# Optimization experiments

Hardware: AMD Instinct MI355X
Metric: run time of the kernel (lower is better)

The kernel has to match this reference:

```python
import jax, jax.numpy as jnp
import numpy as np
from jax import lax

EPS = 1e-5

def binarize(x):
    # sign forward, straight-through (identity) backward, matching torch .data-trick Binarize
    return x + lax.stop_gradient(jnp.sign(x) - x)

def conv2d(x, w, pad):
    return lax.conv_general_dilated(x, w, window_strides=(1, 1),
                                    padding=[(pad, pad), (pad, pad)],
                                    dimension_numbers=('NCHW', 'OIHW', 'NCHW'))

def maxpool_k2s1(x):
    return lax.reduce_window(x, -jnp.inf, lax.max, (1, 1, 2, 2), (1, 1, 1, 1), 'VALID')

def batchnorm(x, g, b):
    # training-mode BN: batch statistics over (N, H, W)
    mean = jnp.mean(x, axis=(0, 2, 3), keepdims=True)
    var = jnp.var(x, axis=(0, 2, 3), keepdims=True)
    return (x - mean) * lax.rsqrt(var + EPS) * g[None, :, None, None] + b[None, :, None, None]

def hardtanh(x):
    return jnp.clip(x, -1.0, 1.0)

def setup_inputs() -> dict:
    key = jax.random.key(0)
    ks = jax.random.split(key, 11)
    B = 4096
    return {
        'x':   jax.random.normal(ks[0], (B, 12, 12, 15), jnp.float32),
        'w1':  jax.random.normal(ks[1], (48, 12, 3, 3), jnp.float32) * 0.1,
        'g1':  1.0 + 0.1 * jax.random.normal(ks[2], (48,), jnp.float32),
        'b1':  0.1 * jax.random.normal(ks[3], (48,), jnp.float32),
        'w2':  jax.random.normal(ks[4], (48, 48, 3, 3), jnp.float32) * 0.1,
        'g2':  1.0 + 0.1 * jax.random.normal(ks[5], (48,), jnp.float32),
        'b2':  0.1 * jax.random.normal(ks[6], (48,), jnp.float32),
        'w3':  jax.random.normal(ks[7], (48, 48, 3, 3), jnp.float32) * 0.1,
        'g3':  1.0 + 0.1 * jax.random.normal(ks[8], (48,), jnp.float32),
        'b3':  0.1 * jax.random.normal(ks[9], (48,), jnp.float32),
        'wfc': jax.random.normal(ks[10], (5, 54 * 48), jnp.float32) * 0.02,
    }

def reference(x, w1, g1, b1, w2, g2, b2, w3, g3, b3, wfc):
    # BinarizeConv2d binarizes activations (in_channels != 3) and weights; returns binarized input too
    xb1 = binarize(x)                                  # [B,12,12,15]
    h = conv2d(xb1, binarize(w1), pad=1)               # [B,48,12,15]
    h = maxpool_k2s1(h)                                # [B,48,11,14]
    h = hardtanh(batchnorm(h, g1, b1))
    xb2 = binarize(h)
    h = conv2d(xb2, binarize(w2), pad=0)               # [B,48,9,12]
    h = hardtanh(batchnorm(h, g2, b2))
    xb3 = binarize(h)
    h = conv2d(xb3, binarize(w3), pad=0)               # [B,48,7,10]
    h = maxpool_k2s1(h)                                # [B,48,6,9] -> 54 spatial
    h = hardtanh(batchnorm(h, g3, b3))
    f = h.reshape(h.shape[0], -1)                      # [B, 2592]
    fb = binarize(f)
    out = fb @ binarize(wfc).T                         # [B, 5]  (LogSoftmax defined but never applied)
    return (out, xb1, xb2, xb3, fb)
```

## Files before the change

### kernel.cpp

```cpp
#include <hip/hip_runtime.h>
#include <stdint.h>

typedef unsigned long long u64;
typedef unsigned short u16;


#define NB 4096

#define WS_STATS 0
#define WS_W1P   20480
#define WS_W2P   24576
#define WS_W3P   28672
#define WS_WFCP  32768
#define WS_A1    40960
#define WS_P1    5111808

#define OUT_OFF 0
#define XB1_OFF 20480
#define XB2_OFF 8867840
#define XB3_OFF 39145472
#define FB_OFF  60379136

__device__ __forceinline__ float fsign(float v) {
    return (v > 0.0f) ? 1.0f : ((v < 0.0f) ? -1.0f : 0.0f);
}

__global__ __launch_bounds__(512)
void kw_pack(const float* __restrict__ w1, const float* __restrict__ w2,
             const float* __restrict__ w3, const float* __restrict__ wfc,
             char* __restrict__ ws) {
    int t = threadIdx.x;
    long long* stats = (long long*)(ws + WS_STATS);
    for (int i = t; i < 2304; i += 512) stats[i] = 0;
    if (t < 432) {
        int oc = t / 9, p = t % 9;
        u16 m1 = 0;
        for (int c = 0; c < 12; ++c)
            if (w1[oc*108 + c*9 + p] > 0.0f) m1 |= (u16)(1u << c);
        ((u16*)(ws + WS_W1P))[t] = m1;
        u64 m2 = 0, m3 = 0;
        for (int c = 0; c < 48; ++c) {
            if (w2[oc*432 + c*9 + p] > 0.0f) m2 |= (1ull << c);
            if (w3[oc*432 + c*9 + p] > 0.0f) m3 |= (1ull << c);
        }
        ((u64*)(ws + WS_W2P))[t] = m2;
        ((u64*)(ws + WS_W3P))[t] = m3;
    }
    if (t < 205) {
        int o = t / 41, j = t % 41;
        u64 m = 0;
        for (int l = 0; l < 64; ++l) {
            int k = j*64 + l;
            if (k < 2592 && wfc[o*2592 + k] > 0.0f) m |= (1ull << l);
        }
        ((u64*)(ws + WS_WFCP))[t] = m;
    }
}

__global__ __launch_bounds__(256)
void k0_binx(const float* __restrict__ x, float* __restrict__ dout,
             char* __restrict__ ws) {
    int id = blockIdx.x*256 + threadIdx.x;
    int b = id / 45, s4 = id % 45;
    const float4* xp = (const float4*)(x + b*2160);
    float4* op = (float4*)(dout + XB1_OFF + (size_t)b*2160);
    u16 m0 = 0, m1 = 0, m2 = 0, m3 = 0;
    #pragma unroll
    for (int c = 0; c < 12; ++c) {
        float4 v = xp[c*45 + s4];
        float4 o;
        o.x = fsign(v.x); o.y = fsign(v.y); o.z = fsign(v.z); o.w = fsign(v.w);
        op[c*45 + s4] = o;
        u16 bit = (u16)(1u << c);
        if (v.x > 0.0f) m0 |= bit;
        if (v.y > 0.0f) m1 |= bit;
        if (v.z > 0.0f) m2 |= bit;
        if (v.w > 0.0f) m3 |= bit;
    }
    ushort4 mm; mm.x = m0; mm.y = m1; mm.z = m2; mm.w = m3;
    *((ushort4*)((u16*)(ws + WS_A1) + b*180 + s4*4)) = mm;
}

__global__ __launch_bounds__(192)
void k1_conv1(char* __restrict__ ws) {
    __shared__ u16 As[180];
    __shared__ signed char cmap[8640];
    __shared__ signed char pl[7392];
    int t = threadIdx.x, b = blockIdx.x;
    const u16* A1 = (const u16*)(ws + WS_A1) + b*180;
    if (t < 180) As[t] = A1[t];
    const u16* __restrict__ W1g = (const u16*)(ws + WS_W1P);
    __syncthreads();
    if (t < 180) {
        int y = t / 15, xx = t % 15;
        u16 tap[9], msk[9];
        int nv = 0;
        #pragma unroll
        for (int ky = 0; ky < 3; ++ky) {
            #pragma unroll
            for (int kx = 0; kx < 3; ++kx) {
                int yy = y + ky - 1, xc = xx + kx - 1;
                bool v = (yy >= 0 && yy < 12 && xc >= 0 && xc < 15);
                int yl = min(max(yy, 0), 11), xl = min(max(xc, 0), 14);
                tap[ky*3+kx] = As[yl*15 + xl];
                msk[ky*3+kx] = v ? (u16)0xFFFF : (u16)0;
                nv += v ? 12 : 0;
            }
        }
        for (int oc = 0; oc < 48; ++oc) {
            int acc = 0;
            #pragma unroll
            for (int k = 0; k < 9; ++k)
                acc += __popc((unsigned)((u16)(tap[k] ^ W1g[oc*9 + k]) & msk[k]));
            cmap[oc*180 + t] = (signed char)(nv - 2*acc);
        }
    }
    __syncthreads();
    signed char* gp = (signed char*)(ws + WS_P1) + (size_t)b*7392;
    for (int i = t; i < 7392; i += 192) {
        int c = i / 154, s = i % 154, py = s / 14, px = s % 14;
        int base = c*180 + py*15 + px;
        int mx = max(max((int)cmap[base],    (int)cmap[base+1]),
                     max((int)cmap[base+15], (int)cmap[base+16]));
        pl[i] = (signed char)mx;
        gp[i] = (signed char)mx;
    }
    __syncthreads();
    int wv = t >> 6, ln = t & 63, slot = b & 7;
    u64* st = (u64*)(ws + WS_STATS);
    for (int c = wv; c < 48; c += 3) {
        int sum = 0, sq = 0;
        for (int s = ln; s < 154; s += 64) {
            int v = pl[c*154 + s];
            sum += v; sq += v*v;
        }
        #pragma unroll
        for (int off = 32; off >= 1; off >>= 1) {
            sum += __shfl_down(sum, off);
            sq  += __shfl_down(sq, off);
        }
        if (ln == 0) {
            atomicAdd(&st[c*8 + slot],        (u64)(long long)sum);
            atomicAdd(&st[(48 + c)*8 + slot], (u64)(long long)sq);
        }
    }
}

__global__ __launch_bounds__(128)
void kA_bn1conv2(const float* __restrict__ g1, const float* __restrict__ b1,
                 float* __restrict__ dout, char* __restrict__ ws) {
    __shared__ float sc[48], sh[48];
    __shared__ int sm_i[1848];
    __shared__ u64 As[154];
    __shared__ short c2s[5184];
    signed char* sm = (signed char*)sm_i;
    int t = threadIdx.x, b = blockIdx.x;
    const int* gp = (const int*)(ws + WS_P1 + (size_t)b*7392);
    for (int i4 = t; i4 < 1848; i4 += 128) sm_i[i4] = gp[i4];
    const u64* __restrict__ W2g = (const u64*)(ws + WS_W2P);
    if (t < 48) {
        const long long* st = (const long long*)(ws + WS_STATS);
        long long s = 0, q = 0;
        #pragma unroll
        for (int k = 0; k < 8; ++k) { s += st[t*8 + k]; q += st[(48 + t)*8 + k]; }
        double N = 630784.0;
        double mean = (double)s / N;
        double var  = (double)q / N - mean*mean;
        double scale = (double)g1[t] / sqrt(var + 1e-5);
        sc[t] = (float)scale;
        sh[t] = (float)((double)b1[t] - mean*scale);
    }
    __syncthreads();
    float4* xo = (float4*)(dout + XB2_OFF + (size_t)b*7392);
    for (int i4 = t; i4 < 1848; i4 += 128) {
        int pv = sm_i[i4];
        int i = i4*4;
        float4 o;
        int c0 = i/154, c1 = (i+1)/154, c2i = (i+2)/154, c3 = (i+3)/154;
        o.x = fsign(sc[c0]*(float)(signed char)(pv)        + sh[c0]);
        o.y = fsign(sc[c1]*(float)(signed char)(pv >> 8)   + sh[c1]);
        o.z = fsign(sc[c2i]*(float)(signed char)(pv >> 16) + sh[c2i]);
        o.w = fsign(sc[c3]*(float)(signed char)(pv >> 24)  + sh[c3]);
        xo[i4] = o;
    }
    u64* A2g = (u64*)(ws + WS_A1) + (size_t)b*154;
    for (int s = t; s < 154; s += 128) {
        u64 m = 0;
        #pragma unroll
        for (int c = 0; c < 48; ++c)
            if (sc[c]*(float)sm[c*154 + s] + sh[c] > 0.0f) m |= (1ull << c);
        As[s] = m;
        A2g[s] = m;
    }
    __syncthreads();
    if (t < 108) {
        int oy = t / 12, ox = t % 12;
        u64 tap[9];
        #pragma unroll
        for (int ky = 0; ky < 3; ++ky)
            #pragma unroll
            for (int kx = 0; kx < 3; ++kx)
                tap[ky*3+kx] = As[(oy+ky)*14 + ox + kx];
        for (int oc = 0; oc < 48; ++oc) {
            int acc = 0;
            #pragma unroll
            for (int k = 0; k < 9; ++k)
                acc += __popcll(tap[k] ^ W2g[oc*9 + k]);
            c2s[oc*108 + t] = (short)(432 - 2*acc);
        }
    }
    __syncthreads();
    int wv = t >> 6, ln = t & 63, slot = b & 7;
    u64* st = (u64*)(ws + WS_STATS);
    for (int c = wv; c < 48; c += 2) {
        int sum = 0, sq = 0;
        for (int s = ln; s < 108; s += 64) {
            int v = c2s[c*108 + s];
            sum += v; sq += v*v;
        }
        #pragma unroll
        for (int off = 32; off >= 1; off >>= 1) {
            sum += __shfl_down(sum, off);
            sq  += __shfl_down(sq, off);
        }
        if (ln == 0) {
            atomicAdd(&st[(96 + c)*8 + slot],  (u64)(long long)sum);
            atomicAdd(&st[(144 + c)*8 + slot], (u64)(long long)sq);
        }
    }
}

__global__ __launch_bounds__(128)
void kB_bn2conv3(const float* __restrict__ g2, const float* __restrict__ b2,
                 float* __restrict__ dout, char* __restrict__ ws) {
    __shared__ float sc[48], sh[48];
    __shared__ u64 As[154];
    __shared__ short c2s[5184];
    __shared__ u64 A3[108];
    __shared__ short cm[3360];
    __shared__ short pls[2592];
    int t = threadIdx.x, b = blockIdx.x;
    const u64* A2g = (const u64*)(ws + WS_A1) + (size_t)b*154;
    for (int s = t; s < 154; s += 128) As[s] = A2g[s];
    const u64* __restrict__ W2g = (const u64*)(ws + WS_W2P);
    const u64* __restrict__ W3g = (const u64*)(ws + WS_W3P);
    if (t < 48) {
        const long long* st = (const long long*)(ws + WS_STATS);
        long long s = 0, q = 0;
        #pragma unroll
        for (int k = 0; k < 8; ++k) { s += st[(96 + t)*8 + k]; q += st[(144 + t)*8 + k]; }
        double N = 442368.0;
        double mean = (double)s / N;
        double var  = (double)q / N - mean*mean;
        double scale = (double)g2[t] / sqrt(var + 1e-5);
        sc[t] = (float)scale;
        sh[t] = (float)((double)b2[t] - mean*scale);
    }
    __syncthreads();
    if (t < 108) {
        int oy = t / 12, ox = t % 12;
        u64 tap[9];
        #pragma unroll
        for (int ky = 0; ky < 3; ++ky)
            #pragma unroll
            for (int kx = 0; kx < 3; ++kx)
                tap[ky*3+kx] = As[(oy+ky)*14 + ox + kx];
        for (int oc = 0; oc < 48; ++oc) {
            int acc = 0;
            #pragma unroll
            for (int k = 0; k < 9; ++k)
                acc += __popcll(tap[k] ^ W2g[oc*9 + k]);
            c2s[oc*108 + t] = (short)(432 - 2*acc);
        }
    }
    __syncthreads();
    float4* xo = (float4*)(dout + XB3_OFF + (size_t)b*5184);
    for (int i4 = t; i4 < 1296; i4 += 128) {
        int c = i4 / 27, s4 = i4 % 27;
        short4 v4 = *(const short4*)&c2s[c*108 + s4*4];
        float4 o;
        o.x = fsign(sc[c]*(float)v4.x + sh[c]);
        o.y = fsign(sc[c]*(float)v4.y + sh[c]);
        o.z = fsign(sc[c]*(float)v4.z + sh[c]);
        o.w = fsign(sc[c]*(float)v4.w + sh[c]);
        xo[i4] = o;
    }
    if (t < 108) {
        u64 m = 0;
        #pragma unroll
        for (int c = 0; c < 48; ++c)
            if (sc[c]*(float)c2s[c*108 + t] + sh[c] > 0.0f) m |= (1ull << c);
        A3[t] = m;
    }
    __syncthreads();
    if (t < 70) {
        int oy = t / 10, ox = t % 10;
        u64 tap[9];
        #pragma unroll
        for (int ky = 0; ky < 3; ++ky)
            #pragma unroll
            for (int kx = 0; kx < 3; ++kx)
                tap[ky*3+kx] = A3[(oy+ky)*12 + ox + kx];
        for (int oc = 0; oc < 48; ++oc) {
            int acc = 0;
            #pragma unroll
            for (int k = 0; k < 9; ++k)
                acc += __popcll(tap[k] ^ W3g[oc*9 + k]);
            cm[oc*70 + t] = (short)(432 - 2*acc);
        }
    }
    __syncthreads();
    short* p3g = (short*)(ws + WS_P1) + (size_t)b*2592;
    for (int i = t; i < 2592; i += 128) {
        int c = i / 54, s = i % 54, py = s / 9, px = s % 9;
        int base = c*70 + py*10 + px;
        int mx = max(max((int)cm[base],    (int)cm[base+1]),
                     max((int)cm[base+10], (int)cm[base+11]));
        pls[i] = (short)mx;
        p3g[i] = (short)mx;
    }
    __syncthreads();
    int wv = t >> 6, ln = t & 63, slot = b & 7;
    u64* st = (u64*)(ws + WS_STATS);
    for (int c = wv; c < 48; c += 2) {
        int sum = 0, sq = 0;
        if (ln < 54) {
            int v = pls[c*54 + ln];
            sum = v; sq = v*v;
        }
        #pragma unroll
        for (int off = 32; off >= 1; off >>= 1) {
            sum += __shfl_down(sum, off);
            sq  += __shfl_down(sq, off);
        }
        if (ln == 0) {
            atomicAdd(&st[(192 + c)*8 + slot], (u64)(long long)sum);
            atomicAdd(&st[(240 + c)*8 + slot], (u64)(long long)sq);
        }
    }
}

__global__ __launch_bounds__(256)
void kC_fbfc(const float* __restrict__ g3, const float* __restrict__ b3,
             float* __restrict__ dout, char* __restrict__ ws) {
    __shared__ float sc[48], sh[48];
    __shared__ short4 sm4[648];
    __shared__ unsigned char nib[648];
    __shared__ u64 fbb[41];
    short* sm = (short*)sm4;
    int t = threadIdx.x, b = blockIdx.x;
    const short4* p3 = (const short4*)((const short*)(ws + WS_P1) + (size_t)b*2592);
    for (int i4 = t; i4 < 648; i4 += 256) sm4[i4] = p3[i4];
    if (t < 48) {
        const long long* st = (const long long*)(ws + WS_STATS);
        long long s = 0, q = 0;
        #pragma unroll
        for (int k = 0; k < 8; ++k) { s += st[(192 + t)*8 + k]; q += st[(240 + t)*8 + k]; }
        double N = 221184.0;
        double mean = (double)s / N;
        double var  = (double)q / N - mean*mean;
        double scale = (double)g3[t] / sqrt(var + 1e-5);
        sc[t] = (float)scale;
        sh[t] = (float)((double)b3[t] - mean*scale);
    }
    __syncthreads();
    float4* fo = (float4*)(dout + FB_OFF + (size_t)b*2592);
    for (int i4 = t; i4 < 648; i4 += 256) {
        int i = i4*4;
        float4 o;
        unsigned n = 0;
        int c0 = i/54, c1 = (i+1)/54, c2 = (i+2)/54, c3 = (i+3)/54;
        float v0 = sc[c0]*(float)sm[i]   + sh[c0];
        float v1 = sc[c1]*(float)sm[i+1] + sh[c1];
        float v2 = sc[c2]*(float)sm[i+2] + sh[c2];
        float v3 = sc[c3]*(float)sm[i+3] + sh[c3];
        o.x = fsign(v0); o.y = fsign(v1); o.z = fsign(v2); o.w = fsign(v3);
        if (v0 > 0.0f) n |= 1u;
        if (v1 > 0.0f) n |= 2u;
        if (v2 > 0.0f) n |= 4u;
        if (v3 > 0.0f) n |= 8u;
        fo[i4] = o;
        nib[i4] = (unsigned char)n;
    }
    __syncthreads();
    if (t < 41) {
        u64 m = 0;
        #pragma unroll
        for (int k = 0; k < 16; ++k) {
            int j = t*16 + k;
            if (j < 648) m |= ((u64)nib[j]) << (4*k);
        }
        fbb[t] = m;
    }
    __syncthreads();
    if (t < 5) {
        const u64* Wf = (const u64*)(ws + WS_WFCP) + t*41;
        int acc = 0;
        #pragma unroll
        for (int j = 0; j < 41; ++j) acc += __popcll(fbb[j] ^ Wf[j]);
        dout[OUT_OFF + b*5 + t] = (float)(2592 - 2*acc);
    }
}

extern "C" void kernel_launch(void* const* d_in, const int* in_sizes, int n_in,
                              void* d_out, int out_size, void* d_ws, size_t ws_size,
                              hipStream_t stream) {
    const float* x   = (const float*)d_in[0];
    const float* w1  = (const float*)d_in[1];
    const float* g1  = (const float*)d_in[2];
    const float* b1  = (const float*)d_in[3];
    const float* w2  = (const float*)d_in[4];
    const float* g2  = (const float*)d_in[5];
    const float* b2  = (const float*)d_in[6];
    const float* w3  = (const float*)d_in[7];
    const float* g3  = (const float*)d_in[8];
    const float* b3  = (const float*)d_in[9];
    const float* wfc = (const float*)d_in[10];
    float* out = (float*)d_out;
    char* ws = (char*)d_ws;

    hipLaunchKernelGGL(kw_pack,     dim3(1),    dim3(512), 0, stream, w1, w2, w3, wfc, ws);
    hipLaunchKernelGGL(k0_binx,     dim3(720),  dim3(256), 0, stream, x, out, ws);
    hipLaunchKernelGGL(k1_conv1,    dim3(NB),   dim3(192), 0, stream, ws);
    hipLaunchKernelGGL(kA_bn1conv2, dim3(NB),   dim3(128), 0, stream, g1, b1, out, ws);
    hipLaunchKernelGGL(kB_bn2conv3, dim3(NB),   dim3(128), 0, stream, g2, b2, out, ws);
    hipLaunchKernelGGL(kC_fbfc,     dim3(NB),   dim3(256), 0, stream, g3, b3, out, ws);
}
```

Measured before the change: 768.5 us.

## Hoist BN constants to tiny kernels, widen blocks, split conv channels across threads

The per-block batch-norm scale/shift computation is moved into separate single-block kernels that write constants to workspace, so each of the 4096 blocks only loads 96 floats instead of redoing double-precision reductions. Conv2/conv3 blocks grow to 256 threads, with output channels split across two or three thread groups so more lanes do popcount work. Pooled outputs are packed and stored as int/int4 words instead of bytes/shorts, and the oc loops get unroll hints. This adds three extra kernel launches and higher per-block register and thread use, which may lower occupancy.

```diff
diff --git a/kernel.cpp b/kernel.cpp
--- a/kernel.cpp
+++ b/kernel.cpp
@@ -4,10 +4,10 @@
 typedef unsigned long long u64;
 typedef unsigned short u16;
 
-
 #define NB 4096
 
 #define WS_STATS 0
+#define WS_CONST 18432
 #define WS_W1P   20480
 #define WS_W2P   24576
 #define WS_W3P   28672
@@ -28,23 +28,23 @@
 __global__ __launch_bounds__(512)
 void kw_pack(const float* __restrict__ w1, const float* __restrict__ w2,
              const float* __restrict__ w3, const float* __restrict__ wfc,
-             char* __restrict__ ws) {
+             u16* __restrict__ W1P, u64* __restrict__ W2P, u64* __restrict__ W3P,
+             u64* __restrict__ WFCP, long long* __restrict__ stats) {
     int t = threadIdx.x;
-    long long* stats = (long long*)(ws + WS_STATS);
     for (int i = t; i < 2304; i += 512) stats[i] = 0;
     if (t < 432) {
         int oc = t / 9, p = t % 9;
         u16 m1 = 0;
         for (int c = 0; c < 12; ++c)
             if (w1[oc*108 + c*9 + p] > 0.0f) m1 |= (u16)(1u << c);
-        ((u16*)(ws + WS_W1P))[t] = m1;
+        W1P[t] = m1;
         u64 m2 = 0, m3 = 0;
         for (int c = 0; c < 48; ++c) {
             if (w2[oc*432 + c*9 + p] > 0.0f) m2 |= (1ull << c);
             if (w3[oc*432 + c*9 + p] > 0.0f) m3 |= (1ull << c);
         }
-        ((u64*)(ws + WS_W2P))[t] = m2;
-        ((u64*)(ws + WS_W3P))[t] = m3;
+        W2P[t] = m2;
+        W3P[t] = m3;
     }
     if (t < 205) {
         int o = t / 41, j = t % 41;
@@ -53,13 +53,30 @@
             int k = j*64 + l;
             if (k < 2592 && wfc[o*2592 + k] > 0.0f) m |= (1ull << l);
         }
-        ((u64*)(ws + WS_WFCP))[t] = m;
+        WFCP[t] = m;
+    }
+}
+
+__global__ __launch_bounds__(64)
+void kbn(const float* __restrict__ g, const float* __restrict__ bb,
+         const long long* __restrict__ st, float* __restrict__ cst, float Nf) {
+    int t = threadIdx.x;
+    if (t < 48) {
+        long long s = 0, q = 0;
+        #pragma unroll
+        for (int k = 0; k < 8; ++k) { s += st[t*8 + k]; q += st[(48 + t)*8 + k]; }
+        double N = (double)Nf;
+        double mean = (double)s / N;
+        double var  = (double)q / N - mean*mean;
+        double scale = (double)g[t] / sqrt(var + 1e-5);
+        cst[t]      = (float)scale;
+        cst[48 + t] = (float)((double)bb[t] - mean*scale);
     }
 }
 
 __global__ __launch_bounds__(256)
 void k0_binx(const float* __restrict__ x, float* __restrict__ dout,
-             char* __restrict__ ws) {
+             u16* __restrict__ A1) {
     int id = blockIdx.x*256 + threadIdx.x;
     int b = id / 45, s4 = id % 45;
     const float4* xp = (const float4*)(x + b*2160);
@@ -78,18 +95,19 @@
         if (v.w > 0.0f) m3 |= bit;
     }
     ushort4 mm; mm.x = m0; mm.y = m1; mm.z = m2; mm.w = m3;
-    *((ushort4*)((u16*)(ws + WS_A1) + b*180 + s4*4)) = mm;
+    *((ushort4*)(A1 + b*180 + s4*4)) = mm;
 }
 
 __global__ __launch_bounds__(192)
-void k1_conv1(char* __restrict__ ws) {
+void k1_conv1(const u16* __restrict__ W1, const u16* __restrict__ A1,
+              int* __restrict__ P1, u64* __restrict__ stats) {
     __shared__ u16 As[180];
-    __shared__ signed char cmap[8640];
-    __shared__ signed char pl[7392];
+    __shared__ int cmap_i[2160];
+    __shared__ int pl_i[1848];
+    signed char* cmap = (signed char*)cmap_i;
+    signed char* pl = (signed char*)pl_i;
     int t = threadIdx.x, b = blockIdx.x;
-    const u16* A1 = (const u16*)(ws + WS_A1) + b*180;
-    if (t < 180) As[t] = A1[t];
-    const u16* __restrict__ W1g = (const u16*)(ws + WS_W1P);
+    if (t < 180) As[t] = A1[b*180 + t];
     __syncthreads();
     if (t < 180) {
         int y = t / 15, xx = t % 15;
@@ -107,27 +125,33 @@
                 nv += v ? 12 : 0;
             }
         }
+        #pragma unroll 4
         for (int oc = 0; oc < 48; ++oc) {
             int acc = 0;
             #pragma unroll
             for (int k = 0; k < 9; ++k)
-                acc += __popc((unsigned)((u16)(tap[k] ^ W1g[oc*9 + k]) & msk[k]));
+                acc += __popc((unsigned)((u16)(tap[k] ^ W1[oc*9 + k]) & msk[k]));
             cmap[oc*180 + t] = (signed char)(nv - 2*acc);
         }
     }
     __syncthreads();
-    signed char* gp = (signed char*)(ws + WS_P1) + (size_t)b*7392;
-    for (int i = t; i < 7392; i += 192) {
-        int c = i / 154, s = i % 154, py = s / 14, px = s % 14;
-        int base = c*180 + py*15 + px;
-        int mx = max(max((int)cmap[base],    (int)cmap[base+1]),
-                     max((int)cmap[base+15], (int)cmap[base+16]));
-        pl[i] = (signed char)mx;
-        gp[i] = (signed char)mx;
+    int* gp = P1 + (size_t)b*1848;
+    for (int i4 = t; i4 < 1848; i4 += 192) {
+        int r = 0;
+        #pragma unroll
+        for (int u = 0; u < 4; ++u) {
+            int i = i4*4 + u;
+            int c = i / 154, s = i % 154, py = s / 14, px = s % 14;
+            int base = c*180 + py*15 + px;
+            int mx = max(max((int)cmap[base],    (int)cmap[base+1]),
+                         max((int)cmap[base+15], (int)cmap[base+16]));
+            r |= (mx & 0xff) << (8*u);
+        }
+        pl_i[i4] = r;
+        gp[i4] = r;
     }
     __syncthreads();
     int wv = t >> 6, ln = t & 63, slot = b & 7;
-    u64* st = (u64*)(ws + WS_STATS);
     for (int c = wv; c < 48; c += 3) {
         int sum = 0, sq = 0;
         for (int s = ln; s < 154; s += 64) {
@@ -140,39 +164,29 @@
             sq  += __shfl_down(sq, off);
         }
         if (ln == 0) {
-            atomicAdd(&st[c*8 + slot],        (u64)(long long)sum);
-            atomicAdd(&st[(48 + c)*8 + slot], (u64)(long long)sq);
-        }
-    }
-}
-
-__global__ __launch_bounds__(128)
-void kA_bn1conv2(const float* __restrict__ g1, const float* __restrict__ b1,
-                 float* __restrict__ dout, char* __restrict__ ws) {
+            atomicAdd((u64*)&stats[c*8 + slot],        (u64)(long long)sum);
+            atomicAdd((u64*)&stats[(48 + c)*8 + slot], (u64)(long long)sq);
+        }
+    }
+}
+
+__global__ __launch_bounds__(256)
+void kA_bn1conv2(const float* __restrict__ cst, const int4* __restrict__ P1,
+                 float* __restrict__ dout, u64* __restrict__ A2,
+                 const u64* __restrict__ W2, u64* __restrict__ stats) {
     __shared__ float sc[48], sh[48];
     __shared__ int sm_i[1848];
     __shared__ u64 As[154];
     __shared__ short c2s[5184];
     signed char* sm = (signed char*)sm_i;
     int t = threadIdx.x, b = blockIdx.x;
-    const int* gp = (const int*)(ws + WS_P1 + (size_t)b*7392);
-    for (int i4 = t; i4 < 1848; i4 += 128) sm_i[i4] = gp[i4];
-    const u64* __restrict__ W2g = (const u64*)(ws + WS_W2P);
-    if (t < 48) {
-        const long long* st = (const long long*)(ws + WS_STATS);
-        long long s = 0, q = 0;
-        #pragma unroll
-        for (int k = 0; k < 8; ++k) { s += st[t*8 + k]; q += st[(48 + t)*8 + k]; }
-        double N = 630784.0;
-        double mean = (double)s / N;
-        double var  = (double)q / N - mean*mean;
-        double scale = (double)g1[t] / sqrt(var + 1e-5);
-        sc[t] = (float)scale;
-        sh[t] = (float)((double)b1[t] - mean*scale);
-    }
+    const int4* gp = P1 + (size_t)b*462;
+    for (int i = t; i < 462; i += 256) ((int4*)sm_i)[i] = gp[i];
+    if (t < 48) sc[t] = cst[t];
+    else if (t < 96) sh[t - 48] = cst[t];
     __syncthreads();
     float4* xo = (float4*)(dout + XB2_OFF + (size_t)b*7392);
-    for (int i4 = t; i4 < 1848; i4 += 128) {
+    for (int i4 = t; i4 < 1848; i4 += 256) {
         int pv = sm_i[i4];
         int i = i4*4;
         float4 o;
@@ -183,36 +197,37 @@
         o.w = fsign(sc[c3]*(float)(signed char)(pv >> 24)  + sh[c3]);
         xo[i4] = o;
     }
-    u64* A2g = (u64*)(ws + WS_A1) + (size_t)b*154;
-    for (int s = t; s < 154; s += 128) {
+    if (t < 154) {
         u64 m = 0;
         #pragma unroll
         for (int c = 0; c < 48; ++c)
-            if (sc[c]*(float)sm[c*154 + s] + sh[c] > 0.0f) m |= (1ull << c);
-        As[s] = m;
-        A2g[s] = m;
-    }
-    __syncthreads();
-    if (t < 108) {
-        int oy = t / 12, ox = t % 12;
+            if (sc[c]*(float)sm[c*154 + t] + sh[c] > 0.0f) m |= (1ull << c);
+        As[t] = m;
+        A2[(size_t)b*154 + t] = m;
+    }
+    __syncthreads();
+    if (t < 216) {
+        int pos = (t < 108) ? t : (t - 108);
+        int ocb = (t < 108) ? 0 : 24;
+        int oy = pos / 12, ox = pos % 12;
         u64 tap[9];
         #pragma unroll
         for (int ky = 0; ky < 3; ++ky)
             #pragma unroll
             for (int kx = 0; kx < 3; ++kx)
                 tap[ky*3+kx] = As[(oy+ky)*14 + ox + kx];
-        for (int oc = 0; oc < 48; ++oc) {
+        #pragma unroll 4
+        for (int oc = ocb; oc < ocb + 24; ++oc) {
             int acc = 0;
             #pragma unroll
             for (int k = 0; k < 9; ++k)
-                acc += __popcll(tap[k] ^ W2g[oc*9 + k]);
-            c2s[oc*108 + t] = (short)(432 - 2*acc);
+                acc += __popcll(tap[k] ^ W2[oc*9 + k]);
+            c2s[oc*108 + pos] = (short)(432 - 2*acc);
         }
     }
     __syncthreads();
     int wv = t >> 6, ln = t & 63, slot = b & 7;
-    u64* st = (u64*)(ws + WS_STATS);
-    for (int c = wv; c < 48; c += 2) {
+    for (int c = wv; c < 48; c += 4) {
         int sum = 0, sq = 0;
         for (int s = ln; s < 108; s += 64) {
             int v = c2s[c*108 + s];
@@ -224,15 +239,17 @@
             sq  += __shfl_down(sq, off);
         }
         if (ln == 0) {
-            atomicAdd(&st[(96 + c)*8 + slot],  (u64)(long long)sum);
-            atomicAdd(&st[(144 + c)*8 + slot], (u64)(long long)sq);
-        }
-    }
-}
-
-__global__ __launch_bounds__(128)
-void kB_bn2conv3(const float* __restrict__ g2, const float* __restrict__ b2,
-                 float* __restrict__ dout, char* __restrict__ ws) {
+            atomicAdd((u64*)&stats[(96 + c)*8 + slot],  (u64)(long long)sum);
+            atomicAdd((u64*)&stats[(144 + c)*8 + slot], (u64)(long long)sq);
+        }
+    }
+}
+
+__global__ __launch_bounds__(256)
+void kB_bn2conv3(const float* __restrict__ cst, const u64* __restrict__ A2,
+                 const u64* __restrict__ W2, const u64* __restrict__ W3,
+                 float* __restrict__ dout, short* __restrict__ P3,
+                 u64* __restrict__ stats) {
     __shared__ float sc[48], sh[48];
     __shared__ u64 As[154];
     __shared__ short c2s[5184];
@@ -240,42 +257,32 @@
     __shared__ short cm[3360];
     __shared__ short pls[2592];
     int t = threadIdx.x, b = blockIdx.x;
-    const u64* A2g = (const u64*)(ws + WS_A1) + (size_t)b*154;
-    for (int s = t; s < 154; s += 128) As[s] = A2g[s];
-    const u64* __restrict__ W2g = (const u64*)(ws + WS_W2P);
-    const u64* __restrict__ W3g = (const u64*)(ws + WS_W3P);
-    if (t < 48) {
-        const long long* st = (const long long*)(ws + WS_STATS);
-        long long s = 0, q = 0;
-        #pragma unroll
-        for (int k = 0; k < 8; ++k) { s += st[(96 + t)*8 + k]; q += st[(144 + t)*8 + k]; }
-        double N = 442368.0;
-        double mean = (double)s / N;
-        double var  = (double)q / N - mean*mean;
-        double scale = (double)g2[t] / sqrt(var + 1e-5);
-        sc[t] = (float)scale;
-        sh[t] = (float)((double)b2[t] - mean*scale);
-    }
-    __syncthreads();
-    if (t < 108) {
-        int oy = t / 12, ox = t % 12;
+    if (t < 154) As[t] = A2[(size_t)b*154 + t];
+    if (t < 48) sc[t] = cst[t];
+    else if (t < 96) sh[t - 48] = cst[t];
+    __syncthreads();
+    if (t < 216) {
+        int pos = (t < 108) ? t : (t - 108);
+        int ocb = (t < 108) ? 0 : 24;
+        int oy = pos / 12, ox = pos % 12;
         u64 tap[9];
         #pragma unroll
         for (int ky = 0; ky < 3; ++ky)
             #pragma unroll
             for (int kx = 0; kx < 3; ++kx)
                 tap[ky*3+kx] = As[(oy+ky)*14 + ox + kx];
-        for (int oc = 0; oc < 48; ++oc) {
+        #pragma unroll 4
+        for (int oc = ocb; oc < ocb + 24; ++oc) {
             int acc = 0;
             #pragma unroll
             for (int k = 0; k < 9; ++k)
-                acc += __popcll(tap[k] ^ W2g[oc*9 + k]);
-            c2s[oc*108 + t] = (short)(432 - 2*acc);
+                acc += __popcll(tap[k] ^ W2[oc*9 + k]);
+            c2s[oc*108 + pos] = (short)(432 - 2*acc);
         }
     }
     __syncthreads();
     float4* xo = (float4*)(dout + XB3_OFF + (size_t)b*5184);
-    for (int i4 = t; i4 < 1296; i4 += 128) {
+    for (int i4 = t; i4 < 1296; i4 += 256) {
         int c = i4 / 27, s4 = i4 % 27;
         short4 v4 = *(const short4*)&c2s[c*108 + s4*4];
         float4 o;
@@ -293,36 +300,48 @@
         A3[t] = m;
     }
     __syncthreads();
-    if (t < 70) {
-        int oy = t / 10, ox = t % 10;
+    if (t < 210) {
+        int grp = (t < 70) ? 0 : ((t < 140) ? 1 : 2);
+        int pos = t - grp*70;
+        int ocb = grp*16;
+        int oy = pos / 10, ox = pos % 10;
         u64 tap[9];
         #pragma unroll
         for (int ky = 0; ky < 3; ++ky)
             #pragma unroll
             for (int kx = 0; kx < 3; ++kx)
                 tap[ky*3+kx] = A3[(oy+ky)*12 + ox + kx];
-        for (int oc = 0; oc < 48; ++oc) {
+        #pragma unroll 4
+        for (int oc = ocb; oc < ocb + 16; ++oc) {
             int acc = 0;
             #pragma unroll
             for (int k = 0; k < 9; ++k)
-                acc += __popcll(tap[k] ^ W3g[oc*9 + k]);
-            cm[oc*70 + t] = (short)(432 - 2*acc);
-        }
-    }
-    __syncthreads();
-    short* p3g = (short*)(ws + WS_P1) + (size_t)b*2592;
-    for (int i = t; i < 2592; i += 128) {
+                acc += __popcll(tap[k] ^ W3[oc*9 + k]);
+            cm[oc*70 + pos] = (short)(432 - 2*acc);
+        }
+    }
+    __syncthreads();
+    int* p3g = (int*)(P3 + (size_t)b*2592);
+    for (int i2 = t; i2 < 1296; i2 += 256) {
+        int i = i2*2;
         int c = i / 54, s = i % 54, py = s / 9, px = s % 9;
         int base = c*70 + py*10 + px;
-        int mx = max(max((int)cm[base],    (int)cm[base+1]),
+        int m0 = max(max((int)cm[base],    (int)cm[base+1]),
                      max((int)cm[base+10], (int)cm[base+11]));
-        pls[i] = (short)mx;
-        p3g[i] = (short)mx;
+        int m1 = max(max((int)cm[base+1],  (int)cm[base+2]),
+                     max((int)cm[base+11], (int)cm[base+12]));
+        if (px == 8) {
+            int base2 = c*70 + (py+1)*10;
+            m1 = max(max((int)cm[base2],    (int)cm[base2+1]),
+                     max((int)cm[base2+10], (int)cm[base2+11]));
+        }
+        pls[i] = (short)m0;
+        pls[i+1] = (short)m1;
+        p3g[i2] = (m0 & 0xffff) | (m1 << 16);
     }
     __syncthreads();
     int wv = t >> 6, ln = t & 63, slot = b & 7;
-    u64* st = (u64*)(ws + WS_STATS);
-    for (int c = wv; c < 48; c += 2) {
+    for (int c = wv; c < 48; c += 4) {
         int sum = 0, sq = 0;
         if (ln < 54) {
             int v = pls[c*54 + ln];
@@ -334,35 +353,25 @@
             sq  += __shfl_down(sq, off);
         }
         if (ln == 0) {
-            atomicAdd(&st[(192 + c)*8 + slot], (u64)(long long)sum);
-            atomicAdd(&st[(240 + c)*8 + slot], (u64)(long long)sq);
+            atomicAdd((u64*)&stats[(192 + c)*8 + slot], (u64)(long long)sum);
+            atomicAdd((u64*)&stats[(240 + c)*8 + slot], (u64)(long long)sq);
         }
     }
 }
 
 __global__ __launch_bounds__(256)
-void kC_fbfc(const float* __restrict__ g3, const float* __restrict__ b3,
-             float* __restrict__ dout, char* __restrict__ ws) {
+void kC_fbfc(const float* __restrict__ cst, const short* __restrict__ P3,
+             const u64* __restrict__ WFC, float* __restrict__ dout) {
     __shared__ float sc[48], sh[48];
     __shared__ short4 sm4[648];
     __shared__ unsigned char nib[648];
     __shared__ u64 fbb[41];
     short* sm = (short*)sm4;
     int t = threadIdx.x, b = blockIdx.x;
-    const short4* p3 = (const short4*)((const short*)(ws + WS_P1) + (size_t)b*2592);
+    const short4* p3 = (const short4*)(P3 + (size_t)b*2592);
     for (int i4 = t; i4 < 648; i4 += 256) sm4[i4] = p3[i4];
-    if (t < 48) {
-        const long long* st = (const long long*)(ws + WS_STATS);
-        long long s = 0, q = 0;
-        #pragma unroll
-        for (int k = 0; k < 8; ++k) { s += st[(192 + t)*8 + k]; q += st[(240 + t)*8 + k]; }
-        double N = 221184.0;
-        double mean = (double)s / N;
-        double var  = (double)q / N - mean*mean;
-        double scale = (double)g3[t] / sqrt(var + 1e-5);
-        sc[t] = (float)scale;
-        sh[t] = (float)((double)b3[t] - mean*scale);
-    }
+    if (t < 48) sc[t] = cst[t];
+    else if (t < 96) sh[t - 48] = cst[t];
     __syncthreads();
     float4* fo = (float4*)(dout + FB_OFF + (size_t)b*2592);
     for (int i4 = t; i4 < 648; i4 += 256) {
@@ -394,7 +403,7 @@
     }
     __syncthreads();
     if (t < 5) {
-        const u64* Wf = (const u64*)(ws + WS_WFCP) + t*41;
+        const u64* Wf = WFC + t*41;
         int acc = 0;
         #pragma unroll
         for (int j = 0; j < 41; ++j) acc += __popcll(fbb[j] ^ Wf[j]);
@@ -419,10 +428,32 @@
     float* out = (float*)d_out;
     char* ws = (char*)d_ws;
 
-    hipLaunchKernelGGL(kw_pack,     dim3(1),    dim3(512), 0, stream, w1, w2, w3, wfc, ws);
-    hipLaunchKernelGGL(k0_binx,     dim3(720),  dim3(256), 0, stream, x, out, ws);
-    hipLaunchKernelGGL(k1_conv1,    dim3(NB),   dim3(192), 0, stream, ws);
-    hipLaunchKernelGGL(kA_bn1conv2, dim3(NB),   dim3(128), 0, stream, g1, b1, out, ws);
-    hipLaunchKernelGGL(kB_bn2conv3, dim3(NB),   dim3(128), 0, stream, g2, b2, out, ws);
-    hipLaunchKernelGGL(kC_fbfc,     dim3(NB),   dim3(256), 0, stream, g3, b3, out, ws);
-}
+    long long* stats = (long long*)(ws + WS_STATS);
+    float*     cst   = (float*)(ws + WS_CONST);
+    u16*       W1P   = (u16*)(ws + WS_W1P);
+    u64*       W2P   = (u64*)(ws + WS_W2P);
+    u64*       W3P   = (u64*)(ws + WS_W3P);
+    u64*       WFCP  = (u64*)(ws + WS_WFCP);
+    u16*       A1    = (u16*)(ws + WS_A1);
+    u64*       A2    = (u64*)(ws + WS_A1);
+    int*       P1    = (int*)(ws + WS_P1);
+    short*     P3    = (short*)(ws + WS_P1);
+
+    hipLaunchKernelGGL(kw_pack,     dim3(1),    dim3(512), 0, stream,
+                       w1, w2, w3, wfc, W1P, W2P, W3P, WFCP, stats);
+    hipLaunchKernelGGL(k0_binx,     dim3(720),  dim3(256), 0, stream, x, out, A1);
+    hipLaunchKernelGGL(k1_conv1,    dim3(NB),   dim3(192), 0, stream,
+                       W1P, A1, P1, (u64*)stats);
+    hipLaunchKernelGGL(kbn,         dim3(1),    dim3(64),  0, stream,
+                       g1, b1, stats, cst, 630784.0f);
+    hipLaunchKernelGGL(kA_bn1conv2, dim3(NB),   dim3(256), 0, stream,
+                       cst, (const int4*)P1, out, A2, W2P, (u64*)stats);
+    hipLaunchKernelGGL(kbn,         dim3(1),    dim3(64),  0, stream,
+                       g2, b2, stats + 96*8, cst + 96, 442368.0f);
+    hipLaunchKernelGGL(kB_bn2conv3, dim3(NB),   dim3(256), 0, stream,
+                       cst + 96, A2, W2P, W3P, out, P3, (u64*)stats);
+    hipLaunchKernelGGL(kbn,         dim3(1),    dim3(64),  0, stream,
+                       g3, b3, stats + 192*8, cst + 192, 221184.0f);
+    hipLaunchKernelGGL(kC_fbfc,     dim3(NB),   dim3(256), 0, stream,
+                       cst + 192, P3, WFCP, out);
+}
```

Result: faster. 720.2 us (-6.3%).
